# Performance work log

Measured on AMD Instinct MI355X. Metric: run time of the kernel, lower is better.

## Reference

```python
import jax, jax.numpy as jnp
import numpy as np

N = 100000   # nodes
E = 1600000  # edges (avg degree 16)
D = 128      # embed_dim
H1, C1 = 8, 16   # gat1: heads=8, out=embed_dim//8=16, concat -> 128
C2 = 32          # gat2: heads=1, out=32
NEG_SLOPE = 0.2  # PyG GATConv default leaky relu slope


def _gat_layer(x, src, dst, W, a_src, a_dst, b, heads, ch, concat):
    """PyG-style GATConv (eval mode, add_self_loops already applied via src/dst)."""
    n = x.shape[0]
    h = (x @ W).reshape(n, heads, ch)                      # [N,H,C]
    alpha_s = jnp.einsum('nhc,hc->nh', h, a_src)           # [N,H]
    alpha_d = jnp.einsum('nhc,hc->nh', h, a_dst)           # [N,H]
    e = jax.nn.leaky_relu(alpha_s[src] + alpha_d[dst], NEG_SLOPE)  # [Etot,H]
    # segment softmax over incoming edges of each dst node
    m = jax.ops.segment_max(e, dst, num_segments=n)        # [N,H]
    ex = jnp.exp(e - m[dst])
    s = jax.ops.segment_sum(ex, dst, num_segments=n)       # [N,H]
    alpha = ex / (s[dst] + 1e-16)                          # [Etot,H]
    out = jax.ops.segment_sum(alpha[:, :, None] * h[src], dst, num_segments=n)  # [N,H,C]
    out = out.reshape(n, heads * ch) if concat else out.mean(axis=1)
    return out + b


def setup_inputs():
    key = jax.random.key(0)
    ks = jax.random.split(key, 12)
    x = jax.random.normal(ks[0], (N, D), dtype=jnp.float32)
    edge_index = jax.random.randint(ks[1], (2, E), 0, N, dtype=jnp.int64)
    sc = 0.1
    W1 = jax.random.normal(ks[2], (D, H1 * C1), jnp.float32) * sc
    a1_src = jax.random.normal(ks[3], (H1, C1), jnp.float32) * sc
    a1_dst = jax.random.normal(ks[4], (H1, C1), jnp.float32) * sc
    b1 = jnp.zeros((H1 * C1,), jnp.float32)
    W2 = jax.random.normal(ks[5], (H1 * C1, C2), jnp.float32) * sc
    a2_src = jax.random.normal(ks[6], (1, C2), jnp.float32) * sc
    a2_dst = jax.random.normal(ks[7], (1, C2), jnp.float32) * sc
    b2 = jnp.zeros((C2,), jnp.float32)
    Wh = jax.random.normal(ks[8], (C2, 1), jnp.float32) * sc
    bh = jnp.zeros((1,), jnp.float32)
    return {"x": x, "edge_index": edge_index,
            "W1": W1, "a1_src": a1_src, "a1_dst": a1_dst, "b1": b1,
            "W2": W2, "a2_src": a2_src, "a2_dst": a2_dst, "b2": b2,
            "Wh": Wh, "bh": bh}


def reference(x, edge_index, W1, a1_src, a1_dst, b1, W2, a2_src, a2_dst, b2, Wh, bh):
    n = x.shape[0]
    loops = jnp.arange(n, dtype=edge_index.dtype)
    src = jnp.concatenate([edge_index[0], loops])  # add_self_loops=True (PyG default)
    dst = jnp.concatenate([edge_index[1], loops])
    h = jax.nn.elu(_gat_layer(x, src, dst, W1, a1_src, a1_dst, b1, H1, C1, True))
    h = jax.nn.elu(_gat_layer(h, src, dst, W2, a2_src, a2_dst, b2, 1, C2, False))
    return h @ Wh + bh  # [N,1] ordinal head
```

## Files before the change

### kernel.cpp

```cpp
#include <hip/hip_runtime.h>
#include <hip/hip_bf16.h>
#include <stdint.h>
#include <stddef.h>

#define NEG_SLOPE 0.2f
#define XS 136

#define NBK   196
#define BWSH  9
#define BCAP  12288
#define NPREP 64

typedef __bf16 bf16x8 __attribute__((ext_vector_type(8)));
typedef float  f32x4  __attribute__((ext_vector_type(4)));

__device__ __forceinline__ float bf2f(__hip_bfloat16 b){ return __bfloat162float(b); }
__device__ __forceinline__ float lo_bf(unsigned u){ return __uint_as_float(u << 16); }
__device__ __forceinline__ float hi_bf(unsigned u){ return __uint_as_float(u & 0xffff0000u); }
__device__ __forceinline__ float lrelu(float u){ return fmaxf(u, NEG_SLOPE * u); }
__device__ __forceinline__ unsigned short f2bf(float f){
    unsigned u = __float_as_uint(f);
    return (unsigned short)((u + 0x7fffu + ((u >> 16) & 1u)) >> 16);
}
__device__ __forceinline__ float bfs2f(unsigned short s){ return __uint_as_float((unsigned)s << 16); }
__device__ __forceinline__ float ldraw(const void* p, int i, int isf){
    return isf ? ((const float*)p)[i] : bf2f(((const __hip_bfloat16*)p)[i]);
}

__global__ void detect_kernel(const unsigned* __restrict__ ei,
                              const unsigned* __restrict__ xw,
                              int* __restrict__ flags,
                              int* __restrict__ gcur){
    __shared__ int vote;
    const int t = threadIdx.x;
    if (t == 0) vote = 0;
    if (t < NBK) gcur[t] = t * BCAP;
    __syncthreads();
    if (t < 64){
        unsigned long long m = __ballot(ei[2*t + 1] != 0u);
        if (t == 0) flags[0] = (m == 0ull) ? 1 : 0;
    }
    {
        unsigned lo = xw[t] & 0xffffu;
        unsigned e  = (lo >> 7) & 0xffu;
        int pl = ((lo & 0x7fffu) == 0u || (e >= 100u && e <= 140u)) ? 1 : 0;
        atomicAdd(&vote, pl);
    }
    __syncthreads();
    if (t == 0) flags[1] = (vote < 128) ? 1 : 0;
}

#define WTS_TOTAL 20993
__global__ __launch_bounds__(256) void prep_scatter_kernel(
        const void* __restrict__ ei, const int* __restrict__ flags,
        int* __restrict__ gcur, unsigned* __restrict__ pairs, int E, int Et, int nsb,
        const void* W1, const void* W2, const void* a1s, const void* a1d,
        const void* b1, const void* a2s, const void* a2d, const void* b2,
        const void* Wh, const void* bh,
        float* __restrict__ w, unsigned short* __restrict__ w1x,
        unsigned short* __restrict__ w2x){
    const int t = threadIdx.x;
    if ((int)blockIdx.x < nsb){
        __shared__ int cnt[NBK], base[NBK], lcnt[NBK];
        const int e0 = blockIdx.x * 4096;
        const int nE = min(4096, Et - e0);
        for (int i = t; i < NBK; i += 256){ cnt[i] = 0; lcnt[i] = 0; }
        __syncthreads();
        const int is64 = flags[0];
        int2 sd[16];
#pragma unroll
        for (int k = 0; k < 16; k++){
            int j = t + k * 256;
            if (j < nE){
                int e = e0 + j, s, d;
                if (e >= E){ s = e - E; d = s; }
                else if (is64){
                    const long long* p = (const long long*)ei;
                    s = (int)p[e]; d = (int)p[(size_t)E + e];
                } else {
                    const int* p = (const int*)ei;
                    s = p[e]; d = p[(size_t)E + e];
                }
                sd[k] = make_int2(s, d);
                atomicAdd(&cnt[d >> BWSH], 1);
            } else sd[k].y = -1;
        }
        __syncthreads();
        for (int b = t; b < NBK; b += 256)
            base[b] = cnt[b] ? atomicAdd(&gcur[b], cnt[b]) : 0;
        __syncthreads();
#pragma unroll
        for (int k = 0; k < 16; k++){
            if (sd[k].y >= 0){
                int b = sd[k].y >> BWSH;
                int r = atomicAdd(&lcnt[b], 1);
                pairs[(size_t)base[b] + r] = ((unsigned)sd[k].x << BWSH) | (unsigned)(sd[k].y & 511);
            }
        }
    } else {
        const int p   = blockIdx.x - nsb;
        const int tid = p * 256 + t;
        const int NT  = NPREP * 256;
        const int isf = flags[1];
        for (int i = tid; i < 513; i += NT){
            int gi = 20480 + i;
            const void* src; int off;
            if      (gi < 20608){ src = a1s; off = gi - 20480; }
            else if (gi < 20736){ src = a1d; off = gi - 20608; }
            else if (gi < 20864){ src = b1;  off = gi - 20736; }
            else if (gi < 20896){ src = a2s; off = gi - 20864; }
            else if (gi < 20928){ src = a2d; off = gi - 20896; }
            else if (gi < 20960){ src = b2;  off = gi - 20928; }
            else if (gi < 20992){ src = Wh;  off = gi - 20960; }
            else                { src = bh;  off = 0; }
            w[gi] = ldraw(src, off, isf);
        }
        for (int i = tid; i < 16384; i += NT){
            int c = i >> 7, k = i & 127;
            w1x[i] = f2bf(ldraw(W1, k*128 + c, isf));
        }
        for (int i = tid; i < 4096; i += NT){
            int c = i >> 7, k = i & 127;
            w2x[i] = f2bf(ldraw(W2, k*32 + c, isf));
        }
        for (int i = tid; i < 12*128; i += NT) w2x[36*128 + i] = 0;
        for (int i = tid; i < 1024; i += NT){
            int h = i >> 7, k = i & 127;
            float ss = 0.f, dd = 0.f;
#pragma unroll
            for (int j = 0; j < 16; j++){
                float hv = ldraw(W1, k*128 + h*16 + j, isf);
                ss += hv * ldraw(a1s, h*16 + j, isf);
                dd += hv * ldraw(a1d, h*16 + j, isf);
            }
            unsigned short sh = f2bf(ss), dh = f2bf(dd);
            w1x[(128+h)*128 + k] = sh;
            w1x[(136+h)*128 + k] = f2bf(ss - bfs2f(sh));
            w1x[(144+h)*128 + k] = dh;
            w1x[(152+h)*128 + k] = f2bf(dd - bfs2f(dh));
        }
        for (int k = tid; k < 128; k += NT){
            float ss = 0.f, dd = 0.f;
#pragma unroll
            for (int j = 0; j < 32; j++){
                float hv = ldraw(W2, k*32 + j, isf);
                ss += hv * ldraw(a2s, j, isf);
                dd += hv * ldraw(a2d, j, isf);
            }
            unsigned short sh = f2bf(ss), dh = f2bf(dd);
            w2x[32*128 + k] = sh;
            w2x[33*128 + k] = f2bf(ss - bfs2f(sh));
            w2x[34*128 + k] = dh;
            w2x[35*128 + k] = f2bf(dd - bfs2f(dh));
        }
    }
}

__global__ __launch_bounds__(256) void g1csr_kernel(
        const unsigned* __restrict__ pairs, const int* __restrict__ gcur,
        int* __restrict__ rowptr, int* __restrict__ csr_src, int Nn,
        const void* __restrict__ xv, const unsigned short* __restrict__ w1x,
        const int* __restrict__ flags, __hip_bfloat16* __restrict__ h1b,
        float* __restrict__ as1, float* __restrict__ ad1){
    __shared__ __align__(16) char smem[52224];
    const int t = threadIdx.x;
    if ((int)blockIdx.x < NBK){
        int* ssz   = (int*)smem;
        int* sscan = ssz + 256;
        int* cnt   = sscan + 256;
        int* sh    = cnt + 512;
        const int b = blockIdx.x;
        int v = (t < NBK) ? (gcur[t] - t * BCAP) : 0;
        ssz[t] = v; sscan[t] = v;
        __syncthreads();
        for (int off = 1; off < 256; off <<= 1){
            int x = (t >= off) ? sscan[t - off] : 0;
            __syncthreads();
            sscan[t] += x;
            __syncthreads();
        }
        const int sz = ssz[b];
        const int eb = (b == 0) ? 0 : sscan[b - 1];
        if (b == 0 && t == 0) rowptr[Nn] = sscan[NBK - 1];
        const unsigned* pp = pairs + (size_t)b * BCAP;
        cnt[t] = 0; cnt[t + 256] = 0;
        __syncthreads();
        for (int i = t; i < sz; i += 256) atomicAdd(&cnt[pp[i] & 511u], 1);
        __syncthreads();
        int l0 = 2*t, l1 = 2*t + 1;
        int s0 = cnt[l0], s1 = cnt[l1], ts = s0 + s1;
        sh[t] = ts; __syncthreads();
        for (int off = 1; off < 256; off <<= 1){
            int x = (t >= off) ? sh[t - off] : 0;
            __syncthreads();
            sh[t] += x;
            __syncthreads();
        }
        int excl = sh[t] - ts;
        __syncthreads();
        cnt[l0] = eb + excl;
        cnt[l1] = eb + excl + s0;
        int n0 = (b << BWSH) + l0, n1 = (b << BWSH) + l1;
        if (n0 < Nn) rowptr[n0] = cnt[l0];
        if (n1 < Nn) rowptr[n1] = cnt[l1];
        __syncthreads();
        for (int i = t; i < sz; i += 256){
            unsigned sd = pp[i];
            int pos = atomicAdd(&cnt[sd & 511u], 1);
            csr_src[pos] = (int)(sd >> BWSH);
        }
    } else {
        __bf16* xls = (__bf16*)smem;
        __bf16* wls = (__bf16*)(smem + 64 * XS * 2);
        const int row0 = ((int)blockIdx.x - NBK) * 64;
        const int n = Nn;

#pragma unroll
        for (int k = 0; k < 8; k++){
            int e = (t + k * 256) * 8;
            int c = e >> 7, kk = e & 127;
            *(uint4*)(&wls[c * XS + kk]) = *(const uint4*)(w1x + e);
        }
        if (row0 + 64 <= n){
            if (flags[1]){
                const float* xp = (const float*)xv + (size_t)row0 * 128;
#pragma unroll
                for (int k = 0; k < 8; k++){
                    int e = (t + k * 256) * 4;
                    int row = e >> 7, col = e & 127;
                    float4 vv = *(const float4*)(xp + e);
                    uint2 o;
                    o.x = (unsigned)f2bf(vv.x) | ((unsigned)f2bf(vv.y) << 16);
                    o.y = (unsigned)f2bf(vv.z) | ((unsigned)f2bf(vv.w) << 16);
                    *(uint2*)(&xls[row * XS + col]) = o;
                }
            } else {
                const unsigned short* xp = (const unsigned short*)xv + (size_t)row0 * 128;
#pragma unroll
                for (int k = 0; k < 4; k++){
                    int e = (t + k * 256) * 8;
                    int row = e >> 7, col = e & 127;
                    *(uint4*)(&xls[row * XS + col]) = *(const uint4*)(xp + e);
                }
            }
        } else {
            const int limit = (n - row0) * 128;
            if (flags[1]){
                const float* xp = (const float*)xv + (size_t)row0 * 128;
                for (int i = t; i < 64 * 128; i += 256){
                    float v = (i < limit) ? xp[i] : 0.f;
                    xls[(i >> 7) * XS + (i & 127)] = (__bf16)v;
                }
            } else {
                const unsigned short* xp = (const unsigned short*)xv + (size_t)row0 * 128;
                for (int i = t; i < 64 * 128; i += 256){
                    unsigned short v = (i < limit) ? xp[i] : (unsigned short)0;
                    ((unsigned short*)xls)[(i >> 7) * XS + (i & 127)] = v;
                }
            }
        }
        __syncthreads();

        const int w    = t >> 6;
        const int lane = t & 63;
        const int l15  = lane & 15;
        const int quad = lane >> 4;

        f32x4 acc[8] = {};
        f32x4 accS = {}, accD = {};
        const __bf16* xbase = &xls[(w * 16 + l15) * XS + quad * 8];
        const __bf16* wbase = &wls[l15 * XS + quad * 8];
        const unsigned short* vsrow = w1x + (128 + l15) * 128 + quad * 8;
        const unsigned short* vdrow = w1x + (144 + l15) * 128 + quad * 8;

#pragma unroll
        for (int ks = 0; ks < 4; ks++){
            bf16x8 af = *(const bf16x8*)(xbase + ks * 32);
#pragma unroll
            for (int tt = 0; tt < 8; tt++){
                bf16x8 bfr = *(const bf16x8*)(wbase + tt * 16 * XS + ks * 32);
                acc[tt] = __builtin_amdgcn_mfma_f32_16x16x32_bf16(af, bfr, acc[tt], 0, 0, 0);
            }
            bf16x8 bS = *(const bf16x8*)(vsrow + ks * 32);
            bf16x8 bD = *(const bf16x8*)(vdrow + ks * 32);
            accS = __builtin_amdgcn_mfma_f32_16x16x32_bf16(af, bS, accS, 0, 0, 0);
            accD = __builtin_amdgcn_mfma_f32_16x16x32_bf16(af, bD, accD, 0, 0, 0);
        }

#pragma unroll
        for (int tt = 0; tt < 8; tt++){
            int col = tt * 16 + l15;
#pragma unroll
            for (int r = 0; r < 4; r++){
                int row = row0 + w * 16 + quad * 4 + r;
                if (row < n) h1b[(size_t)row * 128 + col] = __float2bfloat16(acc[tt][r]);
            }
        }
#pragma unroll
        for (int r = 0; r < 4; r++){
            float vs = accS[r] + __shfl_xor(accS[r], 8);
            float vd = accD[r] + __shfl_xor(accD[r], 8);
            int row = row0 + w * 16 + quad * 4 + r;
            if (l15 < 8 && row < n){
                as1[(size_t)row * 8 + l15] = vs;
                ad1[(size_t)row * 8 + l15] = vd;
            }
        }
    }
}

__global__ __launch_bounds__(256) void gather1_kernel(const int* __restrict__ rowptr,
                                                      const int* __restrict__ csr_src,
                                                      const float* __restrict__ as1,
                                                      const float* __restrict__ ad1,
                                                      const unsigned* __restrict__ h1u,
                                                      const float* __restrict__ b1,
                                                      unsigned* __restrict__ out1u, int n){
    int wid = blockIdx.x * 4 + (threadIdx.x >> 6);
    if (wid >= n) return;
    const int lane = threadIdx.x & 63;
    const int g    = lane >> 3;
    const int h    = lane & 7;
    const int start = rowptr[wid], end = rowptr[wid + 1];
    const float adv = ad1[(size_t)wid * 8 + h];
    float den = 0.f;
    float num[16] = {0.f,0.f,0.f,0.f,0.f,0.f,0.f,0.f,
                     0.f,0.f,0.f,0.f,0.f,0.f,0.f,0.f};
    int j   = start + g;
    int src = (j < end) ? __builtin_nontemporal_load(csr_src + j) : -1;
    const int iters = (end - start + 7) >> 3;
#pragma unroll 2
    for (int it = 0; it < iters; ++it){
        const int jn   = j + 8;
        const int srcn = (jn < end) ? __builtin_nontemporal_load(csr_src + jn) : -1;
        if (src >= 0){
            const unsigned* hp = h1u + (size_t)src * 64 + h * 8;
            uint4 hv0 = *(const uint4*)(hp);
            uint4 hv1 = *(const uint4*)(hp + 4);
            float u = lrelu(as1[src * 8 + h] + adv);
            float w = __expf(u);
            den += w;
            num[0]  += w * lo_bf(hv0.x); num[1]  += w * hi_bf(hv0.x);
            num[2]  += w * lo_bf(hv0.y); num[3]  += w * hi_bf(hv0.y);
            num[4]  += w * lo_bf(hv0.z); num[5]  += w * hi_bf(hv0.z);
            num[6]  += w * lo_bf(hv0.w); num[7]  += w * hi_bf(hv0.w);
            num[8]  += w * lo_bf(hv1.x); num[9]  += w * hi_bf(hv1.x);
            num[10] += w * lo_bf(hv1.y); num[11] += w * hi_bf(hv1.y);
            num[12] += w * lo_bf(hv1.z); num[13] += w * hi_bf(hv1.z);
            num[14] += w * lo_bf(hv1.w); num[15] += w * hi_bf(hv1.w);
        }
        j = jn; src = srcn;
    }
    den += __shfl_xor(den, 8); den += __shfl_xor(den, 16); den += __shfl_xor(den, 32);
#pragma unroll
    for (int k = 0; k < 16; k++){
        num[k] += __shfl_xor(num[k], 8);
        num[k] += __shfl_xor(num[k], 16);
        num[k] += __shfl_xor(num[k], 32);
    }
    if (g == 0){
        const int ch0 = h * 16;
        float inv = 1.f / (den + 1e-16f);
        unsigned op[8];
#pragma unroll
        for (int m = 0; m < 8; m++){
            float r0 = num[2*m]   * inv + b1[ch0 + 2*m];
            float r1 = num[2*m+1] * inv + b1[ch0 + 2*m + 1];
            r0 = r0 > 0.f ? r0 : __expf(r0) - 1.f;
            r1 = r1 > 0.f ? r1 : __expf(r1) - 1.f;
            op[m] = (unsigned)f2bf(r0) | ((unsigned)f2bf(r1) << 16);
        }
        unsigned* ob = out1u + (size_t)wid * 64 + h * 8;
#pragma unroll
        for (int m = 0; m < 4; m++){
            unsigned long long q = (unsigned long long)op[2*m] |
                                   ((unsigned long long)op[2*m+1] << 32);
            __builtin_nontemporal_store(q, (unsigned long long*)(ob + 2*m));
        }
    }
}

__global__ __launch_bounds__(256) void gemm2_kernel(const unsigned* __restrict__ out1u,
                                                    const unsigned short* __restrict__ w2x,
                                                    __hip_bfloat16* __restrict__ h2b,
                                                    float* __restrict__ as2,
                                                    float* __restrict__ ad2, int n){
    __shared__ __align__(16) __bf16 als[64 * XS];
    __shared__ __align__(16) __bf16 wls[32 * XS];
    const int t = threadIdx.x;
    const int row0 = blockIdx.x * 64;

#pragma unroll
    for (int k = 0; k < 2; k++){
        int e = (t + k * 256) * 8;
        int c = e >> 7, kk = e & 127;
        *(uint4*)(&wls[c * XS + kk]) = *(const uint4*)(w2x + e);
    }
    if (row0 + 64 <= n){
#pragma unroll
        for (int k = 0; k < 4; k++){
            int e = (t + k * 256) * 4;
            int row = e >> 6, cu = e & 63;
            *(uint4*)(&((unsigned*)als)[row * 68 + cu]) =
                *(const uint4*)(out1u + (size_t)row0 * 64 + e);
        }
    } else {
        const int limit = (n - row0) * 64;
        for (int i = t; i < 64 * 64; i += 256){
            unsigned v = (i < limit) ? out1u[(size_t)row0 * 64 + i] : 0u;
            ((unsigned*)als)[(i >> 6) * 68 + (i & 63)] = v;
        }
    }
    __syncthreads();

    const int w    = t >> 6;
    const int lane = t & 63;
    const int l15  = lane & 15;
    const int quad = lane >> 4;

    f32x4 acc[2] = {};
    f32x4 accE = {};
    const __bf16* abase = &als[(w * 16 + l15) * XS + quad * 8];
    const __bf16* bbase = &wls[l15 * XS + quad * 8];
    const unsigned short* verow = w2x + (32 + l15) * 128 + quad * 8;

#pragma unroll
    for (int ks = 0; ks < 4; ks++){
        bf16x8 af = *(const bf16x8*)(abase + ks * 32);
#pragma unroll
        for (int tt = 0; tt < 2; tt++){
            bf16x8 bfr = *(const bf16x8*)(bbase + tt * 16 * XS + ks * 32);
            acc[tt] = __builtin_amdgcn_mfma_f32_16x16x32_bf16(af, bfr, acc[tt], 0, 0, 0);
        }
        bf16x8 bE = *(const bf16x8*)(verow + ks * 32);
        accE = __builtin_amdgcn_mfma_f32_16x16x32_bf16(af, bE, accE, 0, 0, 0);
    }

#pragma unroll
    for (int r = 0; r < 4; r++){
        int row = row0 + w * 16 + quad * 4 + r;
        if (row < n){
#pragma unroll
            for (int tt = 0; tt < 2; tt++){
                int col = tt * 16 + l15;
                h2b[(size_t)row * 32 + col] = __float2bfloat16(acc[tt][r]);
            }
        }
        float vE = accE[r] + __shfl_xor(accE[r], 1);
        if (row < n){
            if (l15 == 0) as2[row] = vE;
            if (l15 == 2) ad2[row] = vE;
        }
    }
}

__global__ __launch_bounds__(256) void gather2_kernel(const int* __restrict__ rowptr,
                                                      const int* __restrict__ csr_src,
                                                      const float* __restrict__ as2,
                                                      const float* __restrict__ ad2,
                                                      const unsigned* __restrict__ h2u,
                                                      const float* __restrict__ b2,
                                                      const float* __restrict__ Wh,
                                                      const float* __restrict__ bh,
                                                      const int* __restrict__ flags,
                                                      void* __restrict__ out, int n){
    int wid = blockIdx.x * 4 + (threadIdx.x >> 6);
    if (wid >= n) return;
    const int lane = threadIdx.x & 63;
    const int g = lane >> 2;
    const int c = lane & 3;
    const int start = rowptr[wid], end = rowptr[wid + 1];
    const float adv = ad2[wid];
    float den = 0.f;
    float num[8] = {0.f,0.f,0.f,0.f,0.f,0.f,0.f,0.f};
    int j   = start + g;
    int src = (j < end) ? __builtin_nontemporal_load(csr_src + j) : -1;
    const int iters = (end - start + 15) >> 4;
#pragma unroll 2
    for (int it = 0; it < iters; ++it){
        const int jn   = j + 16;
        const int srcn = (jn < end) ? __builtin_nontemporal_load(csr_src + jn) : -1;
        if (src >= 0){
            uint4 hv = *(const uint4*)(h2u + (size_t)src * 16 + c * 4);
            float u = lrelu(as2[src] + adv);
            float w = __expf(u);
            den += w;
            num[0] += w * lo_bf(hv.x); num[1] += w * hi_bf(hv.x);
            num[2] += w * lo_bf(hv.y); num[3] += w * hi_bf(hv.y);
            num[4] += w * lo_bf(hv.z); num[5] += w * hi_bf(hv.z);
            num[6] += w * lo_bf(hv.w); num[7] += w * hi_bf(hv.w);
        }
        j = jn; src = srcn;
    }
    den += __shfl_xor(den, 4); den += __shfl_xor(den, 8);
    den += __shfl_xor(den, 16); den += __shfl_xor(den, 32);
#pragma unroll
    for (int k = 0; k < 8; k++){
        num[k] += __shfl_xor(num[k], 4);
        num[k] += __shfl_xor(num[k], 8);
        num[k] += __shfl_xor(num[k], 16);
        num[k] += __shfl_xor(num[k], 32);
    }
    float p = 0.f;
    if (g == 0){
        const int ch0 = c * 8;
        float inv = 1.f / (den + 1e-16f);
#pragma unroll
        for (int k = 0; k < 8; k++){
            float v = num[k] * inv + b2[ch0 + k];
            v = v > 0.f ? v : __expf(v) - 1.f;
            p += v * Wh[ch0 + k];
        }
    }
    p += __shfl_xor(p, 1); p += __shfl_xor(p, 2);
    if (lane == 0){
        float r = p + bh[0];
        if (flags[1]) ((float*)out)[wid] = r;
        else          ((__hip_bfloat16*)out)[wid] = __float2bfloat16(r);
    }
}

extern "C" void kernel_launch(void* const* d_in, const int* in_sizes, int n_in,
                              void* d_out, int out_size, void* d_ws, size_t ws_size,
                              hipStream_t stream){
    const void* x   = d_in[0];
    const void* ei  = d_in[1];

    const int Nn = in_sizes[0] / 128;
    const int Ee = in_sizes[1] / 2;
    const int Et = Ee + Nn;
    const int nsb = (Et + 4095) / 4096;

    char* ws = (char*)d_ws;
    auto al = [](size_t v){ return (v + 255) & ~(size_t)255; };
    size_t off = 0;
    int*      flags  = (int*)(ws + off);      off = al(off + 16);
    float*    wts    = (float*)(ws + off);    off = al(off + (size_t)WTS_TOTAL * 4);
    unsigned short* w1x = (unsigned short*)(ws + off); off = al(off + 160 * 128 * 2);
    unsigned short* w2x = (unsigned short*)(ws + off); off = al(off + 48 * 128 * 2);
    int*      gcur   = (int*)(ws + off);      off = al(off + (size_t)NBK * 4);
    int*      rowptr = (int*)(ws + off);      off = al(off + (size_t)(Nn + 1) * 4);
    int*      csrs   = (int*)(ws + off);      off = al(off + (size_t)Et * 4);
    unsigned* pairs  = (unsigned*)(ws + off); off = al(off + (size_t)NBK * BCAP * 4);
    size_t o_h1 = off;
    __hip_bfloat16* h1b = (__hip_bfloat16*)(ws + off); off = al(off + (size_t)Nn * 128 * 2);
    float* as1  = (float*)(ws + off); off = al(off + (size_t)Nn * 8 * 4);
    float* ad1  = (float*)(ws + off); off = al(off + (size_t)Nn * 8 * 4);
    unsigned* out1u = (unsigned*)(ws + off); off = al(off + (size_t)Nn * 128 * 2);
    size_t o2 = o_h1;
    __hip_bfloat16* h2b = (__hip_bfloat16*)(ws + o2); o2 += (size_t)Nn * 32 * 2;
    float* as2  = (float*)(ws + o2);  o2 += (size_t)Nn * 4;
    float* ad2  = (float*)(ws + o2);  o2 += (size_t)Nn * 4;

    float* b1f  = wts + 20736;
    float* b2f  = wts + 20928;
    float* Whf  = wts + 20960;
    float* bhf  = wts + 20992;

    detect_kernel<<<1, 256, 0, stream>>>((const unsigned*)ei, (const unsigned*)x, flags, gcur);

    prep_scatter_kernel<<<nsb + NPREP, 256, 0, stream>>>(ei, flags, gcur, pairs, Ee, Et, nsb,
        d_in[2], d_in[6], d_in[3], d_in[4], d_in[5], d_in[7], d_in[8], d_in[9],
        d_in[10], d_in[11], wts, w1x, w2x);

    g1csr_kernel<<<NBK + (Nn + 63) / 64, 256, 0, stream>>>(pairs, gcur, rowptr, csrs, Nn,
        x, w1x, flags, h1b, as1, ad1);

    gather1_kernel<<<(Nn + 3) / 4, 256, 0, stream>>>(rowptr, csrs, as1, ad1,
                                                     (const unsigned*)h1b, b1f, out1u, Nn);

    gemm2_kernel<<<(Nn + 63) / 64, 256, 0, stream>>>(out1u, w2x, h2b, as2, ad2, Nn);

    gather2_kernel<<<(Nn + 3) / 4, 256, 0, stream>>>(rowptr, csrs, as2, ad2,
                                                     (const unsigned*)h2b, b2f,
                                                     Whf, bhf, flags, d_out, Nn);
}
```

Before: 302.0 us.

## Fuse layer-2 projection into gather1 and reuse scatter ranks

The layer-2 linear projection (W2 plus the attention vectors) is folded into gather1. Each wave writes its ELU'd row to shared memory, and lanes compute the 36 output dot products directly with scalar FMAs. This removes the out1u intermediate round trip through global memory and the separate gemm2 launch, at the cost of per-block W2 staging in shared memory, an extra barrier, and scalar math in place of MFMA. Separately, the scatter kernel reuses the rank returned by the first shared atomic, so the second atomic pass is no longer needed.

```diff
diff --git a/kernel.cpp b/kernel.cpp
--- a/kernel.cpp
+++ b/kernel.cpp
@@ -61,13 +61,14 @@
         unsigned short* __restrict__ w2x){
     const int t = threadIdx.x;
     if ((int)blockIdx.x < nsb){
-        __shared__ int cnt[NBK], base[NBK], lcnt[NBK];
+        __shared__ int cnt[NBK], base[NBK];
         const int e0 = blockIdx.x * 4096;
         const int nE = min(4096, Et - e0);
-        for (int i = t; i < NBK; i += 256){ cnt[i] = 0; lcnt[i] = 0; }
+        for (int i = t; i < NBK; i += 256) cnt[i] = 0;
         __syncthreads();
         const int is64 = flags[0];
         int2 sd[16];
+        int  rk[16];
 #pragma unroll
         for (int k = 0; k < 16; k++){
             int j = t + k * 256;
@@ -82,7 +83,7 @@
                     s = p[e]; d = p[(size_t)E + e];
                 }
                 sd[k] = make_int2(s, d);
-                atomicAdd(&cnt[d >> BWSH], 1);
+                rk[k] = atomicAdd(&cnt[d >> BWSH], 1);
             } else sd[k].y = -1;
         }
         __syncthreads();
@@ -93,8 +94,8 @@
         for (int k = 0; k < 16; k++){
             if (sd[k].y >= 0){
                 int b = sd[k].y >> BWSH;
-                int r = atomicAdd(&lcnt[b], 1);
-                pairs[(size_t)base[b] + r] = ((unsigned)sd[k].x << BWSH) | (unsigned)(sd[k].y & 511);
+                pairs[(size_t)base[b] + rk[k]] =
+                    ((unsigned)sd[k].x << BWSH) | (unsigned)(sd[k].y & 511);
             }
         }
     } else {
@@ -315,14 +316,28 @@
                                                       const float* __restrict__ ad1,
                                                       const unsigned* __restrict__ h1u,
                                                       const float* __restrict__ b1,
-                                                      unsigned* __restrict__ out1u, int n){
-    int wid = blockIdx.x * 4 + (threadIdx.x >> 6);
-    if (wid >= n) return;
-    const int lane = threadIdx.x & 63;
+                                                      const unsigned short* __restrict__ w2x,
+                                                      __hip_bfloat16* __restrict__ h2b,
+                                                      float* __restrict__ as2,
+                                                      float* __restrict__ ad2, int n){
+    __shared__ __align__(16) unsigned short w2s[36 * XS];
+    __shared__ __align__(16) unsigned als[4 * 64];
+    const int t = threadIdx.x;
+    for (int i = t; i < 576; i += 256){
+        int e = i * 8, c = e >> 7, kk = e & 127;
+        *(uint4*)(&w2s[c * XS + kk]) = *(const uint4*)(w2x + e);
+    }
+    const int wv   = t >> 6;
+    const int wid  = blockIdx.x * 4 + wv;
+    const int lane = t & 63;
     const int g    = lane >> 3;
     const int h    = lane & 7;
-    const int start = rowptr[wid], end = rowptr[wid + 1];
-    const float adv = ad1[(size_t)wid * 8 + h];
+    int start = 0, end = 0;
+    float adv = 0.f;
+    if (wid < n){
+        start = rowptr[wid]; end = rowptr[wid + 1];
+        adv = ad1[(size_t)wid * 8 + h];
+    }
     float den = 0.f;
     float num[16] = {0.f,0.f,0.f,0.f,0.f,0.f,0.f,0.f,
                      0.f,0.f,0.f,0.f,0.f,0.f,0.f,0.f};
@@ -358,98 +373,43 @@
         num[k] += __shfl_xor(num[k], 16);
         num[k] += __shfl_xor(num[k], 32);
     }
-    if (g == 0){
+    if (g == 0 && wid < n){
         const int ch0 = h * 16;
         float inv = 1.f / (den + 1e-16f);
-        unsigned op[8];
+        unsigned* ap = als + wv * 64 + h * 8;
 #pragma unroll
         for (int m = 0; m < 8; m++){
             float r0 = num[2*m]   * inv + b1[ch0 + 2*m];
             float r1 = num[2*m+1] * inv + b1[ch0 + 2*m + 1];
             r0 = r0 > 0.f ? r0 : __expf(r0) - 1.f;
             r1 = r1 > 0.f ? r1 : __expf(r1) - 1.f;
-            op[m] = (unsigned)f2bf(r0) | ((unsigned)f2bf(r1) << 16);
-        }
-        unsigned* ob = out1u + (size_t)wid * 64 + h * 8;
-#pragma unroll
-        for (int m = 0; m < 4; m++){
-            unsigned long long q = (unsigned long long)op[2*m] |
-                                   ((unsigned long long)op[2*m+1] << 32);
-            __builtin_nontemporal_store(q, (unsigned long long*)(ob + 2*m));
-        }
-    }
-}
-
-__global__ __launch_bounds__(256) void gemm2_kernel(const unsigned* __restrict__ out1u,
-                                                    const unsigned short* __restrict__ w2x,
-                                                    __hip_bfloat16* __restrict__ h2b,
-                                                    float* __restrict__ as2,
-                                                    float* __restrict__ ad2, int n){
-    __shared__ __align__(16) __bf16 als[64 * XS];
-    __shared__ __align__(16) __bf16 wls[32 * XS];
-    const int t = threadIdx.x;
-    const int row0 = blockIdx.x * 64;
-
-#pragma unroll
-    for (int k = 0; k < 2; k++){
-        int e = (t + k * 256) * 8;
-        int c = e >> 7, kk = e & 127;
-        *(uint4*)(&wls[c * XS + kk]) = *(const uint4*)(w2x + e);
-    }
-    if (row0 + 64 <= n){
-#pragma unroll
-        for (int k = 0; k < 4; k++){
-            int e = (t + k * 256) * 4;
-            int row = e >> 6, cu = e & 63;
-            *(uint4*)(&((unsigned*)als)[row * 68 + cu]) =
-                *(const uint4*)(out1u + (size_t)row0 * 64 + e);
-        }
-    } else {
-        const int limit = (n - row0) * 64;
-        for (int i = t; i < 64 * 64; i += 256){
-            unsigned v = (i < limit) ? out1u[(size_t)row0 * 64 + i] : 0u;
-            ((unsigned*)als)[(i >> 6) * 68 + (i & 63)] = v;
+            ap[m] = (unsigned)f2bf(r0) | ((unsigned)f2bf(r1) << 16);
         }
     }
     __syncthreads();
-
-    const int w    = t >> 6;
-    const int lane = t & 63;
-    const int l15  = lane & 15;
-    const int quad = lane >> 4;
-
-    f32x4 acc[2] = {};
-    f32x4 accE = {};
-    const __bf16* abase = &als[(w * 16 + l15) * XS + quad * 8];
-    const __bf16* bbase = &wls[l15 * XS + quad * 8];
-    const unsigned short* verow = w2x + (32 + l15) * 128 + quad * 8;
-
-#pragma unroll
-    for (int ks = 0; ks < 4; ks++){
-        bf16x8 af = *(const bf16x8*)(abase + ks * 32);
-#pragma unroll
-        for (int tt = 0; tt < 2; tt++){
-            bf16x8 bfr = *(const bf16x8*)(bbase + tt * 16 * XS + ks * 32);
-            acc[tt] = __builtin_amdgcn_mfma_f32_16x16x32_bf16(af, bfr, acc[tt], 0, 0, 0);
-        }
-        bf16x8 bE = *(const bf16x8*)(verow + ks * 32);
-        accE = __builtin_amdgcn_mfma_f32_16x16x32_bf16(af, bE, accE, 0, 0, 0);
-    }
-
-#pragma unroll
-    for (int r = 0; r < 4; r++){
-        int row = row0 + w * 16 + quad * 4 + r;
-        if (row < n){
-#pragma unroll
-            for (int tt = 0; tt < 2; tt++){
-                int col = tt * 16 + l15;
-                h2b[(size_t)row * 32 + col] = __float2bfloat16(acc[tt][r]);
-            }
-        }
-        float vE = accE[r] + __shfl_xor(accE[r], 1);
-        if (row < n){
-            if (l15 == 0) as2[row] = vE;
-            if (l15 == 2) ad2[row] = vE;
+    const int col  = lane;
+    const int nwid = blockIdx.x * 4 + wv;
+    float dot = 0.f;
+    if (col < 36 && nwid < n){
+        const unsigned* av = als + wv * 64;
+        const unsigned short* wr = &w2s[col * XS];
+#pragma unroll
+        for (int k = 0; k < 16; k++){
+            uint4 a  = *(const uint4*)(av + k * 4);
+            uint4 wq = *(const uint4*)(wr + k * 8);
+            dot += lo_bf(a.x)*lo_bf(wq.x) + hi_bf(a.x)*hi_bf(wq.x);
+            dot += lo_bf(a.y)*lo_bf(wq.y) + hi_bf(a.y)*hi_bf(wq.y);
+            dot += lo_bf(a.z)*lo_bf(wq.z) + hi_bf(a.z)*hi_bf(wq.z);
+            dot += lo_bf(a.w)*lo_bf(wq.w) + hi_bf(a.w)*hi_bf(wq.w);
+        }
+    }
+    if (nwid < n){
+        if (col < 32){
+            h2b[(size_t)nwid * 32 + col] = __float2bfloat16(dot);
+        } else if (col < 36){
+            float s = dot + __shfl_xor(dot, 1);
+            if (col == 32) as2[nwid] = s;
+            if (col == 34) ad2[nwid] = s;
         }
     }
 }
@@ -542,15 +502,12 @@
     int*      rowptr = (int*)(ws + off);      off = al(off + (size_t)(Nn + 1) * 4);
     int*      csrs   = (int*)(ws + off);      off = al(off + (size_t)Et * 4);
     unsigned* pairs  = (unsigned*)(ws + off); off = al(off + (size_t)NBK * BCAP * 4);
-    size_t o_h1 = off;
     __hip_bfloat16* h1b = (__hip_bfloat16*)(ws + off); off = al(off + (size_t)Nn * 128 * 2);
     float* as1  = (float*)(ws + off); off = al(off + (size_t)Nn * 8 * 4);
     float* ad1  = (float*)(ws + off); off = al(off + (size_t)Nn * 8 * 4);
-    unsigned* out1u = (unsigned*)(ws + off); off = al(off + (size_t)Nn * 128 * 2);
-    size_t o2 = o_h1;
-    __hip_bfloat16* h2b = (__hip_bfloat16*)(ws + o2); o2 += (size_t)Nn * 32 * 2;
-    float* as2  = (float*)(ws + o2);  o2 += (size_t)Nn * 4;
-    float* ad2  = (float*)(ws + o2);  o2 += (size_t)Nn * 4;
+    __hip_bfloat16* h2b = (__hip_bfloat16*)(ws + off); off = al(off + (size_t)Nn * 32 * 2);
+    float* as2  = (float*)(ws + off); off = al(off + (size_t)Nn * 4);
+    float* ad2  = (float*)(ws + off); off = al(off + (size_t)Nn * 4);
 
     float* b1f  = wts + 20736;
     float* b2f  = wts + 20928;
@@ -567,9 +524,8 @@
         x, w1x, flags, h1b, as1, ad1);
 
     gather1_kernel<<<(Nn + 3) / 4, 256, 0, stream>>>(rowptr, csrs, as1, ad1,
-                                                     (const unsigned*)h1b, b1f, out1u, Nn);
-
-    gemm2_kernel<<<(Nn + 63) / 64, 256, 0, stream>>>(out1u, w2x, h2b, as2, ad2, Nn);
+                                                     (const unsigned*)h1b, b1f,
+                                                     w2x, h2b, as2, ad2, Nn);
 
     gather2_kernel<<<(Nn + 3) / 4, 256, 0, stream>>>(rowptr, csrs, as2, ad2,
                                                      (const unsigned*)h2b, b2f,
```

Result: slower. 341.7 us (+13.1%).
